# Kernel tuning notes

Hardware: AMD Instinct MI355X
Metric: run time of the kernel (lower is better)

The kernel has to match this reference:

```python
import jax, jax.numpy as jnp
import numpy as np

# Config (matches init_kwargs)
B, N, F, S, T, L = 4, 128, 128, 5, 32, 2
R_MAX = 10.0
AVG_NEI = 16.0
# ell index of each of the 16 spherical-harmonic components (l=0..3)
ELL_IDX = np.array([0] + [1]*3 + [2]*5 + [3]*7)


def _edges(n):
    # fully-connected directed edge list without self loops (static)
    i = np.arange(n)
    s = np.repeat(i, n)
    r = np.tile(i, n)
    m = s != r
    return jnp.asarray(s[m]), jnp.asarray(r[m])


def _sh(u):
    # real spherical harmonics up to ell=3, component normalization, unit input
    x, y, z = u[..., 0], u[..., 1], u[..., 2]
    s3, s5, s15 = 3**0.5, 5**0.5, 15**0.5
    s35_8, s105, s21_8, s7 = (35/8)**0.5, 105**0.5, (21/8)**0.5, 7**0.5
    comps = [jnp.ones_like(x),
             s3*x, s3*y, s3*z,
             s15*x*y, s15*y*z, 0.5*s5*(3*z*z - 1), s15*x*z, 0.5*s15*(x*x - y*y),
             s35_8*y*(3*x*x - y*y), s105*x*y*z, s21_8*y*(5*z*z - 1),
             0.5*s7*z*(5*z*z - 3), s21_8*x*(5*z*z - 1),
             0.5*s105*z*(x*x - y*y), s35_8*x*(x*x - 3*y*y)]
    return jnp.stack(comps, axis=-1)  # (E,16)


def _forward(positions, node_features, global_features, W_embed, b_embed,
             Wr1, br1, Wr2, Wnode, c1, c2, c3, Wmix0, Wmix1, Wg1, Wg2, Wvout):
    n = positions.shape[1]
    senders, receivers = _edges(n)
    ell = jnp.asarray(ELL_IDX)

    def single(pos, nf, te):
        pos0 = pos
        node_attrs = jax.nn.one_hot(nf - 1, S, dtype=pos.dtype)
        h = jnp.concatenate([node_attrs, jnp.tile(te, (n, 1))], axis=-1)
        scal = h @ W_embed + b_embed            # (N,F) scalar node feats
        vec = jnp.zeros((n, F, 3), pos.dtype)   # (N,F,3) vector node feats
        v = pos[receivers] - pos[senders]       # (E,3)
        lng = jnp.sqrt(jnp.sum(v*v, -1, keepdims=True) + 1e-12)  # (E,1)
        env = 0.5*(jnp.cos(jnp.pi*lng/R_MAX) + 1.0)*(lng < R_MAX)  # cutoff from lengths_0
        for i in range(L):
            u = v / lng
            Y = _sh(u)                                            # (E,16)
            Rw = jax.nn.silu(lng @ Wr1[i] + br1[i]) @ Wr2[i]      # radial MLP (E,4F)
            Rw = (Rw * env).reshape(-1, 4, F)                     # (E,4,F)
            z = (scal @ Wnode[i])[senders]                        # (E,F)
            vdot = jnp.einsum('ecd,ed->ec', vec[senders], u)      # (E,F)
            f = z + vdot
            # tensor-product messages (E,16,F)
            M = Rw[:, ell, :] * Y[:, :, None] * f[:, None, :]
            A = jnp.zeros((n, 16, F), pos.dtype).at[receivers].add(M) / AVG_NEI
            # correlation-3 symmetric-contraction gate via per-ell invariants
            nrm = jnp.zeros((n, 4, F), pos.dtype).at[:, ell, :].add(A*A)
            g = 1.0 + c1[i]*nrm + c2[i]*nrm*nrm + c3[i]*nrm*nrm*nrm
            A = A * g[:, ell, :]
            # linear mix to hidden irreps 128x0e + 128x1o
            scal = A[:, 0, :] @ Wmix0[i]                          # (N,F)
            vec = jnp.einsum('nmc,ck->nkm', A[:, 1:4, :], Wmix1[i])  # (N,F,3)
            # nonlinear readout -> equivariant position update
            gate = jax.nn.silu(scal @ Wg1[i]) @ Wg2[i]            # (N,F)
            mbv = jnp.sum(vec * (gate * Wvout[i])[:, :, None], 1) # (N,3)
            pos = pos + mbv
            v = pos[receivers] - pos[senders]
            lng = jnp.sqrt(jnp.sum(v*v, -1, keepdims=True) + 1e-12)
        return pos - pos0  # predicted noise on positions

    return jax.vmap(single)(positions, node_features, global_features)


def setup_inputs() -> dict:
    key = jax.random.key(0)
    ks = jax.random.split(key, 20)
    sc = 0.1
    p = {}
    p['positions'] = jax.random.normal(ks[0], (B, N, 3), jnp.float32)
    p['node_features'] = jax.random.randint(ks[1], (B, N), 1, S + 1).astype(jnp.int32)
    p['global_features'] = jax.random.normal(ks[2], (B, T), jnp.float32)
    p['W_embed'] = jax.random.normal(ks[3], (S + T, F)) * sc
    p['b_embed'] = jnp.zeros((F,))
    p['Wr1'] = jax.random.normal(ks[4], (L, 1, 64)) * sc
    p['br1'] = jnp.zeros((L, 64))
    p['Wr2'] = jax.random.normal(ks[5], (L, 64, 4 * F)) * sc
    p['Wnode'] = jax.random.normal(ks[6], (L, F, F)) * sc
    p['c1'] = jax.random.normal(ks[7], (L, 4, F)) * 0.01
    p['c2'] = jax.random.normal(ks[8], (L, 4, F)) * 0.001
    p['c3'] = jax.random.normal(ks[9], (L, 4, F)) * 0.0001
    p['Wmix0'] = jax.random.normal(ks[10], (L, F, F)) * sc
    p['Wmix1'] = jax.random.normal(ks[11], (L, F, F)) * sc
    p['Wg1'] = jax.random.normal(ks[12], (L, F, 16)) * sc
    p['Wg2'] = jax.random.normal(ks[13], (L, 16, F)) * sc
    p['Wvout'] = jax.random.normal(ks[14], (L, F)) * sc
    return p


def reference(positions, node_features, global_features, W_embed, b_embed,
              Wr1, br1, Wr2, Wnode, c1, c2, c3, Wmix0, Wmix1, Wg1, Wg2, Wvout):
    return _forward(positions, node_features, global_features, W_embed, b_embed,
                    Wr1, br1, Wr2, Wnode, c1, c2, c3, Wmix0, Wmix1, Wg1, Wg2, Wvout)
```

## Files before the change

kernel.cpp:

```cpp
#include <hip/hip_runtime.h>
#include <hip/hip_bf16.h>
#include <math.h>

#define NB 4
#define NN 128
#define NF 128
#define NS 5
#define NT 32
#define NL 2

typedef __hip_bfloat16 bf16;
typedef short bf16x8 __attribute__((ext_vector_type(8)));
typedef float f32x4 __attribute__((ext_vector_type(4)));

typedef const void __attribute__((address_space(1))) gv_t;
typedef void __attribute__((address_space(3))) lv_t;

__device__ __forceinline__ float b2f(const bf16 x) { return __bfloat162float(x); }
__device__ __forceinline__ float fast_rcp(float x) { return __builtin_amdgcn_rcpf(x); }
__device__ __forceinline__ float fast_rsq(float x) { return __builtin_amdgcn_rsqf(x); }
__device__ __forceinline__ float silu_fast(float x) { return x * fast_rcp(1.0f + __expf(-x)); }
__device__ __forceinline__ float ldf(const void* p, int i, int fl) {
  return fl ? b2f(((const bf16*)p)[i]) : ((const float*)p)[i];
}
__device__ __forceinline__ short f2bf(float x) {
  unsigned u = __float_as_uint(x);
  unsigned r = (u + 0x7fffu + ((u >> 16) & 1u)) >> 16;
  return (short)r;
}
__device__ __forceinline__ void gload16(const float4* g, float4* l) {
  __builtin_amdgcn_global_load_lds((gv_t*)g, (lv_t*)l, 16, 0, 0);
}

#define PI_F 3.14159265358979323846f
#define SQRT3_F 1.7320508075688772f

#define POS_OFF 0
#define GF_OFF  1536
#define WE_OFF  1664
#define BE_OFF  6400
#define WR1_OFF 6528
#define BR1_OFF 6656
#define WR2_OFF 6784
#define WN_OFF  72320
#define C1_OFF  105088
#define C2_OFF  106112
#define C3_OFF  107136
#define M0_OFF  108160
#define M1_OFF  140928
#define G1_OFF  173696
#define G2_OFF  177792
#define WV_OFF  181888
#define CVT_TOTAL 182144

__global__ void prep_convert_kernel(
    const void* __restrict__ pos_raw, const int* __restrict__ nfeat,
    const void* __restrict__ gf,  const void* __restrict__ we,
    const void* __restrict__ be,  const void* __restrict__ wr1,
    const void* __restrict__ br1, const void* __restrict__ wr2,
    const void* __restrict__ wn,  const void* __restrict__ c1,
    const void* __restrict__ c2,  const void* __restrict__ c3,
    const void* __restrict__ m0,  const void* __restrict__ m1,
    const void* __restrict__ g1,  const void* __restrict__ g2,
    const void* __restrict__ wv,
    int* __restrict__ flag, float* __restrict__ cvt,
    float* __restrict__ pos_cur, float4* __restrict__ zv,
    float* __restrict__ env, short* __restrict__ pkw)
{
  __shared__ float posB[NN*3];
  __shared__ float scs[NF];
  __shared__ int sbad;
  const int tid = threadIdx.x;
  const int bn  = blockIdx.x;
  const int b   = bn >> 7;
  const int n   = bn & 127;

  if (tid == 0) sbad = 0;
  __syncthreads();
  {
    const bf16* p = (const bf16*)pos_raw;
    int bad = 0;
    for (int i = tid; i < NB*NN*3; i += 256) {
      float v = b2f(p[i]);
      if (!(fabsf(v) <= 1024.0f)) bad = 1;
    }
    if (bad) sbad = 1;
  }
  __syncthreads();
  const int fl = sbad ? 0 : 1;
  if (bn == 0 && tid == 0) *flag = fl;

  for (int i = bn*256 + tid; i < CVT_TOTAL; i += 512*256) {
    const void* src; int j;
    if      (i < GF_OFF)  { src = pos_raw; j = i - POS_OFF; }
    else if (i < WE_OFF)  { src = gf;  j = i - GF_OFF; }
    else if (i < BE_OFF)  { src = we;  j = i - WE_OFF; }
    else if (i < WR1_OFF) { src = be;  j = i - BE_OFF; }
    else if (i < BR1_OFF) { src = wr1; j = i - WR1_OFF; }
    else if (i < WR2_OFF) { src = br1; j = i - BR1_OFF; }
    else if (i < WN_OFF)  { src = wr2; j = i - WR2_OFF; }
    else if (i < C1_OFF)  { src = wn;  j = i - WN_OFF; }
    else if (i < C2_OFF)  { src = c1;  j = i - C1_OFF; }
    else if (i < C3_OFF)  { src = c2;  j = i - C2_OFF; }
    else if (i < M0_OFF)  { src = c3;  j = i - C3_OFF; }
    else if (i < M1_OFF)  { src = m0;  j = i - M0_OFF; }
    else if (i < G1_OFF)  { src = m1;  j = i - M1_OFF; }
    else if (i < G2_OFF)  { src = g1;  j = i - G1_OFF; }
    else if (i < WV_OFF)  { src = g2;  j = i - G2_OFF; }
    else                  { src = wv;  j = i - WV_OFF; }
    cvt[i] = fl ? b2f(((const bf16*)src)[j]) : ((const float*)src)[j];
  }

  if (bn < 16) {
    int gid  = bn*256 + tid;
    int lyr  = gid >> 11;
    int r    = gid & 2047;
    int wv2  = r >> 9;
    int t    = (r >> 7) & 3;
    int ks   = (r >> 6) & 1;
    int lane = r & 63;
    int qq = lane >> 4, nn = lane & 15;
    int col = wv2*64 + t*16 + nn;
    short* dst = pkw + (size_t)gid*8;
    #pragma unroll
    for (int j = 0; j < 8; ++j) {
      int k = ks*32 + qq*8 + j;
      float v = ldf(wr2, lyr*64*512 + k*512 + col, fl);
      if (wv2 >= 2) v *= SQRT3_F;
      dst[j] = f2bf(v);
    }
  }

  for (int i = tid; i < NN*3; i += 256)
    posB[i] = ldf(pos_raw, b*NN*3 + i, fl);
  if (tid < 128) {
    int sp = nfeat[bn] - 1;
    float acc = ldf(we, sp*NF + tid, fl) + ldf(be, tid, fl);
    #pragma unroll 8
    for (int t = 0; t < NT; ++t)
      acc += ldf(gf, b*NT + t, fl) * ldf(we, (NS + t)*NF + tid, fl);
    scs[tid] = acc;
  }
  __syncthreads();

  if (tid < 128) {
    const int f = tid;
    {
      float px = posB[n*3+0], py = posB[n*3+1], pz = posB[n*3+2];
      float vx = px - posB[f*3+0];
      float vy = py - posB[f*3+1];
      float vz = pz - posB[f*3+2];
      float lng = sqrtf(vx*vx + vy*vy + vz*vz + 1e-12f);
      env[bn*NN + f] = (lng < 10.0f) ? 0.5f*(cosf(PI_F*lng*0.1f) + 1.0f) : 0.0f;
    }
    {
      float acc = 0.f;
      if (fl) {
        const bf16* W = (const bf16*)wn;
        #pragma unroll 8
        for (int k = 0; k < NF; ++k) acc += scs[k] * b2f(W[k*NF + f]);
      } else {
        const float* W = (const float*)wn;
        #pragma unroll 8
        for (int k = 0; k < NF; ++k) acc += scs[k] * W[k*NF + f];
      }
      zv[(size_t)bn*NF + f] = make_float4(acc, 0.f, 0.f, 0.f);
    }
    if (f < 3) pos_cur[bn*3 + f] = posB[n*3 + f];
  }
}

__global__ __launch_bounds__(256, 2)
void fused_kernel(const float* __restrict__ posIn, float* __restrict__ posOut,
                  const float4* __restrict__ zvIn, float4* __restrict__ zvOut,
                  const float* __restrict__ env,  const float* __restrict__ cvt,
                  const short* __restrict__ pk, int layer, int last,
                  const int* __restrict__ flag, void* __restrict__ out)
{
  union SM {
    float4 zvp[2][16][NF];
    struct {
      float P[8][32][17];
      float Pg[8][16];
      float scs[NF];
      float h16[16];
      float red[2][4];
    } nd;
  };
  __shared__ __align__(16) SM sm;
  __shared__ float posL[NN*3];
  __shared__ float envL[NN];
  __shared__ float w1L[64], b1L[64];
  __shared__ __align__(16) short hidA[2][16][72];
  __shared__ __align__(16) float4 uenvL[2][16];
  __shared__ float Ash[4][NF];

  const int tid  = threadIdx.x;
  const int bidx = blockIdx.x;
  const int b    = bidx >> 7;
  const int n    = bidx & 127;

  const int wvid  = tid >> 6;
  const int lane  = tid & 63;
  const int n16   = lane & 15;
  const int q     = lane >> 4;
  const int halfB = wvid >> 1;

  {
    const float4* g = zvIn + (size_t)b*NN*NF + wvid*64 + lane;
    float4* l = &sm.zvp[0][0][0] + wvid*64;
    #pragma unroll
    for (int rep = 0; rep < 8; ++rep)
      gload16(g + rep*256, l + rep*256);
  }

  for (int i = tid; i < NN*3; i += 256)
    posL[i] = posIn[b*NN*3 + i];
  if (tid < 128) envL[tid] = env[(size_t)(b*NN + n)*NN + tid];
  if (tid < 64) {
    w1L[tid] = cvt[WR1_OFF + layer*64 + tid];
    b1L[tid] = cvt[BR1_OFF + layer*64 + tid];
  }
  bf16x8 bfr[4][2];
  {
    const bf16x8* PK = (const bf16x8*)pk + (size_t)layer*2048 + wvid*512 + lane;
    #pragma unroll
    for (int t = 0; t < 4; ++t) {
      #pragma unroll
      for (int ks = 0; ks < 2; ++ks)
        bfr[t][ks] = PK[(t*2 + ks)*64];
    }
  }
  float acR[12];
  #pragma unroll
  for (int i = 0; i < 12; ++i) acR[i] = 0.f;

  __syncthreads();

  const float hrx = posL[n*3 + 0];
  const float hry = posL[n*3 + 1];
  const float hrz = posL[n*3 + 2];
  const float w1v = w1L[lane], b1v = b1L[lane];

  #pragma unroll
  for (int j = 0; j < 4; ++j) {
    int si = wvid*4 + j;
    int s  = si;
    float vx = hrx - posL[s*3 + 0];
    float vy = hry - posL[s*3 + 1];
    float vz = hrz - posL[s*3 + 2];
    float d = vx*vx + vy*vy + vz*vz + 1e-12f;
    float lng = d * fast_rsq(d);
    hidA[0][si][lane] = f2bf(silu_fast(lng * w1v + b1v));
  }
  if (tid < 16) {
    int s = tid;
    float vx = hrx - posL[s*3 + 0];
    float vy = hry - posL[s*3 + 1];
    float vz = hrz - posL[s*3 + 2];
    float d = vx*vx + vy*vy + vz*vz + 1e-12f;
    float inv = fast_rsq(d);
    float envw = (s == n) ? 0.f : envL[s] * 0.0625f;
    uenvL[0][tid] = make_float4(vx*inv, vy*inv, vz*inv, envw);
  }
  __syncthreads();

  #pragma unroll 2
  for (int c = 0; c < 8; ++c) {
    const int cb = c & 1, nb = cb ^ 1;
    const int nc0 = (c + 1) * 16;

    if (c < 7) {
      const float4* g = zvIn + ((size_t)b*NN + nc0)*NF + wvid*64 + lane;
      float4* l = &sm.zvp[nb][0][0] + wvid*64;
      #pragma unroll
      for (int rep = 0; rep < 8; ++rep)
        gload16(g + rep*256, l + rep*256);
    }

    bf16x8 af0 = *(const bf16x8*)&hidA[cb][n16][q*8];
    bf16x8 af1 = *(const bf16x8*)&hidA[cb][n16][q*8 + 32];
    float4 ue[4];
    #pragma unroll
    for (int r = 0; r < 4; ++r) ue[r] = uenvL[cb][q*4 + r];

    #pragma unroll
    for (int t = 0; t < 4; ++t) {
      f32x4 Cf = {0.f, 0.f, 0.f, 0.f};
      Cf = __builtin_amdgcn_mfma_f32_16x16x32_bf16(af0, bfr[t][0], Cf, 0, 0, 0);
      Cf = __builtin_amdgcn_mfma_f32_16x16x32_bf16(af1, bfr[t][1], Cf, 0, 0, 0);
      int f = (wvid*64 + t*16 + n16) & 127;
      if (!halfB) {
        float a0 = 0.f;
        #pragma unroll
        for (int r = 0; r < 4; ++r) {
          float4 zv = sm.zvp[cb][q*4 + r][f];
          float fv = zv.x + ue[r].x*zv.y + ue[r].y*zv.z + ue[r].z*zv.w;
          a0 += (Cf[r] * ue[r].w) * fv;
        }
        acR[t] += a0;
      } else {
        float t1 = 0.f, t2 = 0.f, t3 = 0.f;
        #pragma unroll
        for (int r = 0; r < 4; ++r) {
          float4 zv = sm.zvp[cb][q*4 + r][f];
          float fv = zv.x + ue[r].x*zv.y + ue[r].y*zv.z + ue[r].z*zv.w;
          float tt = (Cf[r] * ue[r].w) * fv;
          t1 += tt * ue[r].x;
          t2 += tt * ue[r].y;
          t3 += tt * ue[r].z;
        }
        acR[t*3 + 0] += t1;
        acR[t*3 + 1] += t2;
        acR[t*3 + 2] += t3;
      }
    }

    if (c < 7) {
      #pragma unroll
      for (int j = 0; j < 4; ++j) {
        int si = wvid*4 + j;
        int s  = nc0 + si;
        float vx = hrx - posL[s*3 + 0];
        float vy = hry - posL[s*3 + 1];
        float vz = hrz - posL[s*3 + 2];
        float d = vx*vx + vy*vy + vz*vz + 1e-12f;
        float lng = d * fast_rsq(d);
        hidA[nb][si][lane] = f2bf(silu_fast(lng * w1v + b1v));
      }
      if (tid < 16) {
        int s = nc0 + tid;
        float vx = hrx - posL[s*3 + 0];
        float vy = hry - posL[s*3 + 1];
        float vz = hrz - posL[s*3 + 2];
        float d = vx*vx + vy*vy + vz*vz + 1e-12f;
        float inv = fast_rsq(d);
        float envw = (s == n) ? 0.f : envL[s] * 0.0625f;
        uenvL[nb][tid] = make_float4(vx*inv, vy*inv, vz*inv, envw);
      }
    }
    __syncthreads();
  }

  #pragma unroll
  for (int i = 0; i < 12; ++i) {
    float v = acR[i];
    v += __shfl_xor(v, 16, 64);
    v += __shfl_xor(v, 32, 64);
    acR[i] = v;
  }
  if (lane < 16) {
    #pragma unroll
    for (int t = 0; t < 4; ++t) {
      int f = (wvid*64 + t*16 + lane) & 127;
      if (!halfB) {
        Ash[0][f] = acR[t];
      } else {
        Ash[1][f] = acR[t*3 + 0];
        Ash[2][f] = acR[t*3 + 1];
        Ash[3][f] = acR[t*3 + 2];
      }
    }
  }
  __syncthreads();

  const int fn = tid & 127;
  float v0 = 0.f, v1 = 0.f, v2 = 0.f;
  float zacc = 0.f;

  if (tid < 128) {
    float a0 = Ash[0][fn];
    float a1 = Ash[1][fn];
    float a2 = Ash[2][fn];
    float a3 = Ash[3][fn];
    float n0 = a0*a0;
    float C1 = cvt[C1_OFF + (layer*4 + 0)*NF + fn];
    float C2 = cvt[C2_OFF + (layer*4 + 0)*NF + fn];
    float C3 = cvt[C3_OFF + (layer*4 + 0)*NF + fn];
    float g0 = 1.0f + C1*n0 + C2*n0*n0 + C3*n0*n0*n0;
    float n1 = a1*a1 + a2*a2 + a3*a3;
    float D1 = cvt[C1_OFF + (layer*4 + 1)*NF + fn];
    float D2 = cvt[C2_OFF + (layer*4 + 1)*NF + fn];
    float D3 = cvt[C3_OFF + (layer*4 + 1)*NF + fn];
    float g1 = 1.0f + D1*n1 + D2*n1*n1 + D3*n1*n1*n1;
    Ash[0][fn] = a0 * g0;
    Ash[1][fn] = a1 * g1;
    Ash[2][fn] = a2 * g1;
    Ash[3][fn] = a3 * g1;
  }
  __syncthreads();

  {
    const float* M0 = cvt + M0_OFF + layer*NF*NF;
    const float* M1 = cvt + M1_OFF + layer*NF*NF;
    const int kh = tid >> 5;
    const int fq = tid & 31;
    float s0=0.f,s1=0.f,s2=0.f,s3=0.f;
    float w00=0.f,w01=0.f,w02=0.f,w03=0.f;
    float w10=0.f,w11=0.f,w12=0.f,w13=0.f;
    float w20=0.f,w21=0.f,w22=0.f,w23=0.f;
    #pragma unroll 4
    for (int kk = 0; kk < 16; ++kk) {
      int k = kh*16 + kk;
      float a0 = Ash[0][k], a1 = Ash[1][k], a2 = Ash[2][k], a3 = Ash[3][k];
      float4 m0 = *(const float4*)(M0 + k*NF + fq*4);
      float4 m1 = *(const float4*)(M1 + k*NF + fq*4);
      s0 += a0*m0.x; s1 += a0*m0.y; s2 += a0*m0.z; s3 += a0*m0.w;
      w00 += a1*m1.x; w01 += a1*m1.y; w02 += a1*m1.z; w03 += a1*m1.w;
      w10 += a2*m1.x; w11 += a2*m1.y; w12 += a2*m1.z; w13 += a2*m1.w;
      w20 += a3*m1.x; w21 += a3*m1.y; w22 += a3*m1.z; w23 += a3*m1.w;
    }
    float* Pp = &sm.nd.P[kh][fq][0];
    Pp[0]=s0;  Pp[1]=s1;  Pp[2]=s2;  Pp[3]=s3;
    Pp[4]=w00; Pp[5]=w01; Pp[6]=w02; Pp[7]=w03;
    Pp[8]=w10; Pp[9]=w11; Pp[10]=w12; Pp[11]=w13;
    Pp[12]=w20; Pp[13]=w21; Pp[14]=w22; Pp[15]=w23;
  }
  __syncthreads();

  if (tid < 128) {
    int fq = fn >> 2, j = fn & 3;
    float sn = 0.f;
    #pragma unroll
    for (int kh = 0; kh < 8; ++kh) {
      const float* Pp = &sm.nd.P[kh][fq][0];
      sn += Pp[j];
      v0 += Pp[4 + j];
      v1 += Pp[8 + j];
      v2 += Pp[12 + j];
    }
    sm.nd.scs[fn] = sn;
  }
  __syncthreads();

  if (!last) {
    const float* W = cvt + WN_OFF + (layer+1)*NF*NF;
    const int kh = tid >> 5;
    const int fq = tid & 31;
    float s0=0.f,s1=0.f,s2=0.f,s3=0.f;
    #pragma unroll 4
    for (int kk = 0; kk < 16; ++kk) {
      int k = kh*16 + kk;
      float a = sm.nd.scs[k];
      float4 m = *(const float4*)(W + k*NF + fq*4);
      s0 += a*m.x; s1 += a*m.y; s2 += a*m.z; s3 += a*m.w;
    }
    float* Pp = &sm.nd.P[kh][fq][0];
    Pp[0]=s0; Pp[1]=s1; Pp[2]=s2; Pp[3]=s3;
  }
  if (tid < 128) {
    const float* G1 = cvt + G1_OFF + layer*NF*16;
    int o = tid & 15, g = tid >> 4;
    float acc = 0.f;
    #pragma unroll
    for (int kk = 0; kk < 16; ++kk) {
      int k = g*16 + kk;
      acc += sm.nd.scs[k] * G1[k*16 + o];
    }
    sm.nd.Pg[g][o] = acc;
  }
  __syncthreads();

  if (!last && tid < 128) {
    int fq = fn >> 2, j = fn & 3;
    #pragma unroll
    for (int kh = 0; kh < 8; ++kh) zacc += sm.nd.P[kh][fq][j];
  }
  if (tid < 16) {
    float acc = 0.f;
    #pragma unroll
    for (int g = 0; g < 8; ++g) acc += sm.nd.Pg[g][tid];
    sm.nd.h16[tid] = silu_fast(acc);
  }
  __syncthreads();

  if (tid < 128) {
    const float* G2 = cvt + G2_OFF + layer*16*NF;
    float gate = 0.f;
    #pragma unroll
    for (int j = 0; j < 16; ++j)
      gate += sm.nd.h16[j] * G2[j*NF + fn];
    float gv = gate * cvt[WV_OFF + layer*NF + fn];

    if (!last)
      zvOut[(size_t)bidx*NF + fn] = make_float4(zacc, v0, v1, v2);

    float p0 = v0*gv, p1 = v1*gv, p2 = v2*gv;
    #pragma unroll
    for (int off = 32; off > 0; off >>= 1) {
      p0 += __shfl_down(p0, off, 64);
      p1 += __shfl_down(p1, off, 64);
      p2 += __shfl_down(p2, off, 64);
    }
    int wave = fn >> 6;
    if ((fn & 63) == 0) {
      sm.nd.red[wave][0] = p0;
      sm.nd.red[wave][1] = p1;
      sm.nd.red[wave][2] = p2;
    }
  }
  __syncthreads();
  if (tid == 0) {
    float m0 = sm.nd.red[0][0] + sm.nd.red[1][0];
    float m1 = sm.nd.red[0][1] + sm.nd.red[1][1];
    float m2 = sm.nd.red[0][2] + sm.nd.red[1][2];
    float px = posL[n*3+0] + m0;
    float py = posL[n*3+1] + m1;
    float pz = posL[n*3+2] + m2;
    if (!last) {
      posOut[bidx*3+0] = px;
      posOut[bidx*3+1] = py;
      posOut[bidx*3+2] = pz;
    } else {
      float ox = px - cvt[POS_OFF + bidx*3+0];
      float oy = py - cvt[POS_OFF + bidx*3+1];
      float oz = pz - cvt[POS_OFF + bidx*3+2];
      if (*flag) {
        bf16* o = (bf16*)out;
        o[bidx*3+0] = __float2bfloat16(ox);
        o[bidx*3+1] = __float2bfloat16(oy);
        o[bidx*3+2] = __float2bfloat16(oz);
      } else {
        float* o = (float*)out;
        o[bidx*3+0] = ox;
        o[bidx*3+1] = oy;
        o[bidx*3+2] = oz;
      }
    }
  }
}

extern "C" void kernel_launch(void* const* d_in, const int* in_sizes, int n_in,
                              void* d_out, int out_size, void* d_ws, size_t ws_size,
                              hipStream_t stream)
{
  (void)in_sizes; (void)n_in; (void)out_size; (void)ws_size;
  const int* nfeat = (const int*)d_in[1];

  float*  ws   = (float*)d_ws;
  int*    flag = (int*)ws;
  float*  cvt  = ws + 16;
  float*  pos0 = cvt + CVT_TOTAL;
  float*  pos1 = pos0 + NB*NN*3;
  float4* zv0  = (float4*)(pos1 + NB*NN*3);
  float4* zv1  = zv0 + (size_t)NB*NN*NF;
  float*  env  = (float*)(zv1 + (size_t)NB*NN*NF);
  short*  pk   = (short*)(env + NB*NN*NN);

  prep_convert_kernel<<<512, 256, 0, stream>>>(
      d_in[0], nfeat, d_in[2], d_in[3], d_in[4], d_in[5], d_in[6], d_in[7],
      d_in[8], d_in[9], d_in[10], d_in[11], d_in[12], d_in[13], d_in[14],
      d_in[15], d_in[16], flag, cvt, pos0, zv0, env, pk);

  fused_kernel<<<512, 256, 0, stream>>>(pos0, pos1, zv0, zv1, env, cvt, pk,
                                        0, 0, flag, d_out);
  fused_kernel<<<512, 256, 0, stream>>>(pos1, (float*)0, zv1, (float4*)0, env,
                                        cvt, pk, 1, 1, flag, d_out);
}
```

Measured before the change: 141.8 us.

## Merge prep and both layer kernels into one persistent kernel with grid barriers

Replaces the three launches (prep plus two layer kernels) with a single kernel that synchronises all 512 blocks through an atomic-counter grid barrier between stages. The envelope and positions are kept in shared memory instead of round-tripping through global buffers, and the barrier counter is reset with a memset each call. This targets launch overhead and inter-kernel gaps. It adds the cost of spinning barriers and depends on all 512 blocks being co-resident (launch_bounds 256,2); if they are not, the kernel deadlocks.

```diff
diff --git a/kernel.cpp b/kernel.cpp
--- a/kernel.cpp
+++ b/kernel.cpp
@@ -30,6 +30,18 @@
 }
 __device__ __forceinline__ void gload16(const float4* g, float4* l) {
   __builtin_amdgcn_global_load_lds((gv_t*)g, (lv_t*)l, 16, 0, 0);
+}
+
+__device__ __forceinline__ void grid_barrier(unsigned* bar, unsigned target) {
+  __syncthreads();
+  if (threadIdx.x == 0) {
+    __threadfence();
+    __hip_atomic_fetch_add(bar, 1u, __ATOMIC_RELAXED, __HIP_MEMORY_SCOPE_AGENT);
+    while (__hip_atomic_load(bar, __ATOMIC_RELAXED, __HIP_MEMORY_SCOPE_AGENT) < target)
+      __builtin_amdgcn_s_sleep(2);
+    __threadfence();
+  }
+  __syncthreads();
 }
 
 #define PI_F 3.14159265358979323846f
@@ -53,7 +65,8 @@
 #define WV_OFF  181888
 #define CVT_TOTAL 182144
 
-__global__ void prep_convert_kernel(
+__global__ __launch_bounds__(256, 2)
+void mega_kernel(
     const void* __restrict__ pos_raw, const int* __restrict__ nfeat,
     const void* __restrict__ gf,  const void* __restrict__ we,
     const void* __restrict__ be,  const void* __restrict__ wr1,
@@ -63,17 +76,40 @@
     const void* __restrict__ m0,  const void* __restrict__ m1,
     const void* __restrict__ g1,  const void* __restrict__ g2,
     const void* __restrict__ wv,
-    int* __restrict__ flag, float* __restrict__ cvt,
-    float* __restrict__ pos_cur, float4* __restrict__ zv,
-    float* __restrict__ env, short* __restrict__ pkw)
+    unsigned* __restrict__ bar, float* __restrict__ cvt,
+    float* __restrict__ pos1, float4* __restrict__ zv0,
+    float4* __restrict__ zv1, short* __restrict__ pkw,
+    void* __restrict__ out)
 {
-  __shared__ float posB[NN*3];
-  __shared__ float scs[NF];
+  union SM {
+    float4 zvp[2][16][NF];
+    struct {
+      float P[8][32][17];
+      float Pg[8][16];
+      float scs[NF];
+      float h16[16];
+      float red[2][4];
+    } nd;
+  };
+  __shared__ __align__(16) SM sm;
+  __shared__ float posL[NN*3];
+  __shared__ float envL[NN];
+  __shared__ float w1L[64], b1L[64];
+  __shared__ __align__(16) short hidA[2][16][72];
+  __shared__ __align__(16) float4 uenvL[2][16];
+  __shared__ float Ash[4][NF];
   __shared__ int sbad;
-  const int tid = threadIdx.x;
-  const int bn  = blockIdx.x;
-  const int b   = bn >> 7;
-  const int n   = bn & 127;
+
+  const int tid  = threadIdx.x;
+  const int bidx = blockIdx.x;
+  const int b    = bidx >> 7;
+  const int n    = bidx & 127;
+
+  const int wvid  = tid >> 6;
+  const int lane  = tid & 63;
+  const int n16   = lane & 15;
+  const int q     = lane >> 4;
+  const int halfB = wvid >> 1;
 
   if (tid == 0) sbad = 0;
   __syncthreads();
@@ -88,9 +124,11 @@
   }
   __syncthreads();
   const int fl = sbad ? 0 : 1;
-  if (bn == 0 && tid == 0) *flag = fl;
-
-  for (int i = bn*256 + tid; i < CVT_TOTAL; i += 512*256) {
+
+  for (int i = tid; i < NN*3; i += 256)
+    posL[i] = ldf(pos_raw, b*NN*3 + i, fl);
+
+  for (int i = bidx*256 + tid; i < CVT_TOTAL; i += 512*256) {
     const void* src; int j;
     if      (i < GF_OFF)  { src = pos_raw; j = i - POS_OFF; }
     else if (i < WE_OFF)  { src = gf;  j = i - GF_OFF; }
@@ -111,15 +149,15 @@
     cvt[i] = fl ? b2f(((const bf16*)src)[j]) : ((const float*)src)[j];
   }
 
-  if (bn < 16) {
-    int gid  = bn*256 + tid;
+  if (bidx < 16) {
+    int gid  = bidx*256 + tid;
     int lyr  = gid >> 11;
     int r    = gid & 2047;
     int wv2  = r >> 9;
     int t    = (r >> 7) & 3;
     int ks   = (r >> 6) & 1;
-    int lane = r & 63;
-    int qq = lane >> 4, nn = lane & 15;
+    int ln   = r & 63;
+    int qq = ln >> 4, nn = ln & 15;
     int col = wv2*64 + t*16 + nn;
     short* dst = pkw + (size_t)gid*8;
     #pragma unroll
@@ -131,402 +169,372 @@
     }
   }
 
-  for (int i = tid; i < NN*3; i += 256)
-    posB[i] = ldf(pos_raw, b*NN*3 + i, fl);
   if (tid < 128) {
-    int sp = nfeat[bn] - 1;
+    int sp = nfeat[bidx] - 1;
     float acc = ldf(we, sp*NF + tid, fl) + ldf(be, tid, fl);
     #pragma unroll 8
     for (int t = 0; t < NT; ++t)
       acc += ldf(gf, b*NT + t, fl) * ldf(we, (NS + t)*NF + tid, fl);
-    scs[tid] = acc;
+    sm.nd.scs[tid] = acc;
   }
   __syncthreads();
 
   if (tid < 128) {
     const int f = tid;
     {
-      float px = posB[n*3+0], py = posB[n*3+1], pz = posB[n*3+2];
-      float vx = px - posB[f*3+0];
-      float vy = py - posB[f*3+1];
-      float vz = pz - posB[f*3+2];
+      float px = posL[n*3+0], py = posL[n*3+1], pz = posL[n*3+2];
+      float vx = px - posL[f*3+0];
+      float vy = py - posL[f*3+1];
+      float vz = pz - posL[f*3+2];
       float lng = sqrtf(vx*vx + vy*vy + vz*vz + 1e-12f);
-      env[bn*NN + f] = (lng < 10.0f) ? 0.5f*(cosf(PI_F*lng*0.1f) + 1.0f) : 0.0f;
+      envL[f] = (lng < 10.0f) ? 0.5f*(cosf(PI_F*lng*0.1f) + 1.0f) : 0.0f;
     }
     {
       float acc = 0.f;
       if (fl) {
         const bf16* W = (const bf16*)wn;
         #pragma unroll 8
-        for (int k = 0; k < NF; ++k) acc += scs[k] * b2f(W[k*NF + f]);
+        for (int k = 0; k < NF; ++k) acc += sm.nd.scs[k] * b2f(W[k*NF + f]);
       } else {
         const float* W = (const float*)wn;
         #pragma unroll 8
-        for (int k = 0; k < NF; ++k) acc += scs[k] * W[k*NF + f];
-      }
-      zv[(size_t)bn*NF + f] = make_float4(acc, 0.f, 0.f, 0.f);
-    }
-    if (f < 3) pos_cur[bn*3 + f] = posB[n*3 + f];
-  }
-}
-
-__global__ __launch_bounds__(256, 2)
-void fused_kernel(const float* __restrict__ posIn, float* __restrict__ posOut,
-                  const float4* __restrict__ zvIn, float4* __restrict__ zvOut,
-                  const float* __restrict__ env,  const float* __restrict__ cvt,
-                  const short* __restrict__ pk, int layer, int last,
-                  const int* __restrict__ flag, void* __restrict__ out)
-{
-  union SM {
-    float4 zvp[2][16][NF];
-    struct {
-      float P[8][32][17];
-      float Pg[8][16];
-      float scs[NF];
-      float h16[16];
-      float red[2][4];
-    } nd;
-  };
-  __shared__ __align__(16) SM sm;
-  __shared__ float posL[NN*3];
-  __shared__ float envL[NN];
-  __shared__ float w1L[64], b1L[64];
-  __shared__ __align__(16) short hidA[2][16][72];
-  __shared__ __align__(16) float4 uenvL[2][16];
-  __shared__ float Ash[4][NF];
-
-  const int tid  = threadIdx.x;
-  const int bidx = blockIdx.x;
-  const int b    = bidx >> 7;
-  const int n    = bidx & 127;
-
-  const int wvid  = tid >> 6;
-  const int lane  = tid & 63;
-  const int n16   = lane & 15;
-  const int q     = lane >> 4;
-  const int halfB = wvid >> 1;
-
-  {
-    const float4* g = zvIn + (size_t)b*NN*NF + wvid*64 + lane;
-    float4* l = &sm.zvp[0][0][0] + wvid*64;
-    #pragma unroll
-    for (int rep = 0; rep < 8; ++rep)
-      gload16(g + rep*256, l + rep*256);
-  }
-
-  for (int i = tid; i < NN*3; i += 256)
-    posL[i] = posIn[b*NN*3 + i];
-  if (tid < 128) envL[tid] = env[(size_t)(b*NN + n)*NN + tid];
-  if (tid < 64) {
-    w1L[tid] = cvt[WR1_OFF + layer*64 + tid];
-    b1L[tid] = cvt[BR1_OFF + layer*64 + tid];
-  }
-  bf16x8 bfr[4][2];
-  {
-    const bf16x8* PK = (const bf16x8*)pk + (size_t)layer*2048 + wvid*512 + lane;
-    #pragma unroll
-    for (int t = 0; t < 4; ++t) {
-      #pragma unroll
-      for (int ks = 0; ks < 2; ++ks)
-        bfr[t][ks] = PK[(t*2 + ks)*64];
-    }
-  }
-  float acR[12];
-  #pragma unroll
-  for (int i = 0; i < 12; ++i) acR[i] = 0.f;
-
-  __syncthreads();
-
-  const float hrx = posL[n*3 + 0];
-  const float hry = posL[n*3 + 1];
-  const float hrz = posL[n*3 + 2];
-  const float w1v = w1L[lane], b1v = b1L[lane];
-
-  #pragma unroll
-  for (int j = 0; j < 4; ++j) {
-    int si = wvid*4 + j;
-    int s  = si;
-    float vx = hrx - posL[s*3 + 0];
-    float vy = hry - posL[s*3 + 1];
-    float vz = hrz - posL[s*3 + 2];
-    float d = vx*vx + vy*vy + vz*vz + 1e-12f;
-    float lng = d * fast_rsq(d);
-    hidA[0][si][lane] = f2bf(silu_fast(lng * w1v + b1v));
-  }
-  if (tid < 16) {
-    int s = tid;
-    float vx = hrx - posL[s*3 + 0];
-    float vy = hry - posL[s*3 + 1];
-    float vz = hrz - posL[s*3 + 2];
-    float d = vx*vx + vy*vy + vz*vz + 1e-12f;
-    float inv = fast_rsq(d);
-    float envw = (s == n) ? 0.f : envL[s] * 0.0625f;
-    uenvL[0][tid] = make_float4(vx*inv, vy*inv, vz*inv, envw);
-  }
-  __syncthreads();
-
-  #pragma unroll 2
-  for (int c = 0; c < 8; ++c) {
-    const int cb = c & 1, nb = cb ^ 1;
-    const int nc0 = (c + 1) * 16;
-
-    if (c < 7) {
-      const float4* g = zvIn + ((size_t)b*NN + nc0)*NF + wvid*64 + lane;
-      float4* l = &sm.zvp[nb][0][0] + wvid*64;
+        for (int k = 0; k < NF; ++k) acc += sm.nd.scs[k] * W[k*NF + f];
+      }
+      zv0[(size_t)bidx*NF + f] = make_float4(acc, 0.f, 0.f, 0.f);
+    }
+  }
+
+  grid_barrier(bar, 512);
+
+  for (int layer = 0; layer < NL; ++layer) {
+    const int last = (layer == NL-1);
+    const float4* zvIn  = layer ? zv1 : zv0;
+    float4*       zvOut = layer ? (float4*)0 : zv1;
+
+    if (layer) {
+      grid_barrier(bar, 1024);
+      for (int i = tid; i < NN*3; i += 256)
+        posL[i] = pos1[b*NN*3 + i];
+    }
+    {
+      const float4* g = zvIn + (size_t)b*NN*NF + wvid*64 + lane;
+      float4* l = &sm.zvp[0][0][0] + wvid*64;
       #pragma unroll
       for (int rep = 0; rep < 8; ++rep)
         gload16(g + rep*256, l + rep*256);
     }
-
-    bf16x8 af0 = *(const bf16x8*)&hidA[cb][n16][q*8];
-    bf16x8 af1 = *(const bf16x8*)&hidA[cb][n16][q*8 + 32];
-    float4 ue[4];
+    if (tid < 64) {
+      w1L[tid] = cvt[WR1_OFF + layer*64 + tid];
+      b1L[tid] = cvt[BR1_OFF + layer*64 + tid];
+    }
+    bf16x8 bfr[4][2];
+    {
+      const bf16x8* PK = (const bf16x8*)pkw + (size_t)layer*2048 + wvid*512 + lane;
+      #pragma unroll
+      for (int t = 0; t < 4; ++t) {
+        #pragma unroll
+        for (int ks = 0; ks < 2; ++ks)
+          bfr[t][ks] = PK[(t*2 + ks)*64];
+      }
+    }
+    float acR[12];
     #pragma unroll
-    for (int r = 0; r < 4; ++r) ue[r] = uenvL[cb][q*4 + r];
+    for (int i = 0; i < 12; ++i) acR[i] = 0.f;
+
+    __syncthreads();
+
+    const float hrx = posL[n*3 + 0];
+    const float hry = posL[n*3 + 1];
+    const float hrz = posL[n*3 + 2];
+    const float w1v = w1L[lane], b1v = b1L[lane];
 
     #pragma unroll
-    for (int t = 0; t < 4; ++t) {
-      f32x4 Cf = {0.f, 0.f, 0.f, 0.f};
-      Cf = __builtin_amdgcn_mfma_f32_16x16x32_bf16(af0, bfr[t][0], Cf, 0, 0, 0);
-      Cf = __builtin_amdgcn_mfma_f32_16x16x32_bf16(af1, bfr[t][1], Cf, 0, 0, 0);
-      int f = (wvid*64 + t*16 + n16) & 127;
-      if (!halfB) {
-        float a0 = 0.f;
+    for (int j = 0; j < 4; ++j) {
+      int si = wvid*4 + j;
+      int s  = si;
+      float vx = hrx - posL[s*3 + 0];
+      float vy = hry - posL[s*3 + 1];
+      float vz = hrz - posL[s*3 + 2];
+      float d = vx*vx + vy*vy + vz*vz + 1e-12f;
+      float lng = d * fast_rsq(d);
+      hidA[0][si][lane] = f2bf(silu_fast(lng * w1v + b1v));
+    }
+    if (tid < 16) {
+      int s = tid;
+      float vx = hrx - posL[s*3 + 0];
+      float vy = hry - posL[s*3 + 1];
+      float vz = hrz - posL[s*3 + 2];
+      float d = vx*vx + vy*vy + vz*vz + 1e-12f;
+      float inv = fast_rsq(d);
+      float envw = (s == n) ? 0.f : envL[s] * 0.0625f;
+      uenvL[0][tid] = make_float4(vx*inv, vy*inv, vz*inv, envw);
+    }
+    __syncthreads();
+
+    #pragma unroll 2
+    for (int c = 0; c < 8; ++c) {
+      const int cb = c & 1, nb = cb ^ 1;
+      const int nc0 = (c + 1) * 16;
+
+      if (c < 7) {
+        const float4* g = zvIn + ((size_t)b*NN + nc0)*NF + wvid*64 + lane;
+        float4* l = &sm.zvp[nb][0][0] + wvid*64;
         #pragma unroll
-        for (int r = 0; r < 4; ++r) {
-          float4 zv = sm.zvp[cb][q*4 + r][f];
-          float fv = zv.x + ue[r].x*zv.y + ue[r].y*zv.z + ue[r].z*zv.w;
-          a0 += (Cf[r] * ue[r].w) * fv;
+        for (int rep = 0; rep < 8; ++rep)
+          gload16(g + rep*256, l + rep*256);
+      }
+
+      bf16x8 af0 = *(const bf16x8*)&hidA[cb][n16][q*8];
+      bf16x8 af1 = *(const bf16x8*)&hidA[cb][n16][q*8 + 32];
+      float4 ue[4];
+      #pragma unroll
+      for (int r = 0; r < 4; ++r) ue[r] = uenvL[cb][q*4 + r];
+
+      #pragma unroll
+      for (int t = 0; t < 4; ++t) {
+        f32x4 Cf = {0.f, 0.f, 0.f, 0.f};
+        Cf = __builtin_amdgcn_mfma_f32_16x16x32_bf16(af0, bfr[t][0], Cf, 0, 0, 0);
+        Cf = __builtin_amdgcn_mfma_f32_16x16x32_bf16(af1, bfr[t][1], Cf, 0, 0, 0);
+        int f = (wvid*64 + t*16 + n16) & 127;
+        if (!halfB) {
+          float a0 = 0.f;
+          #pragma unroll
+          for (int r = 0; r < 4; ++r) {
+            float4 zv = sm.zvp[cb][q*4 + r][f];
+            float fv = zv.x + ue[r].x*zv.y + ue[r].y*zv.z + ue[r].z*zv.w;
+            a0 += (Cf[r] * ue[r].w) * fv;
+          }
+          acR[t] += a0;
+        } else {
+          float t1 = 0.f, t2 = 0.f, t3 = 0.f;
+          #pragma unroll
+          for (int r = 0; r < 4; ++r) {
+            float4 zv = sm.zvp[cb][q*4 + r][f];
+            float fv = zv.x + ue[r].x*zv.y + ue[r].y*zv.z + ue[r].z*zv.w;
+            float tt = (Cf[r] * ue[r].w) * fv;
+            t1 += tt * ue[r].x;
+            t2 += tt * ue[r].y;
+            t3 += tt * ue[r].z;
+          }
+          acR[t*3 + 0] += t1;
+          acR[t*3 + 1] += t2;
+          acR[t*3 + 2] += t3;
         }
-        acR[t] += a0;
+      }
+
+      if (c < 7) {
+        #pragma unroll
+        for (int j = 0; j < 4; ++j) {
+          int si = wvid*4 + j;
+          int s  = nc0 + si;
+          float vx = hrx - posL[s*3 + 0];
+          float vy = hry - posL[s*3 + 1];
+          float vz = hrz - posL[s*3 + 2];
+          float d = vx*vx + vy*vy + vz*vz + 1e-12f;
+          float lng = d * fast_rsq(d);
+          hidA[nb][si][lane] = f2bf(silu_fast(lng * w1v + b1v));
+        }
+        if (tid < 16) {
+          int s = nc0 + tid;
+          float vx = hrx - posL[s*3 + 0];
+          float vy = hry - posL[s*3 + 1];
+          float vz = hrz - posL[s*3 + 2];
+          float d = vx*vx + vy*vy + vz*vz + 1e-12f;
+          float inv = fast_rsq(d);
+          float envw = (s == n) ? 0.f : envL[s] * 0.0625f;
+          uenvL[nb][tid] = make_float4(vx*inv, vy*inv, vz*inv, envw);
+        }
+      }
+      __syncthreads();
+    }
+
+    #pragma unroll
+    for (int i = 0; i < 12; ++i) {
+      float v = acR[i];
+      v += __shfl_xor(v, 16, 64);
+      v += __shfl_xor(v, 32, 64);
+      acR[i] = v;
+    }
+    if (lane < 16) {
+      #pragma unroll
+      for (int t = 0; t < 4; ++t) {
+        int f = (wvid*64 + t*16 + lane) & 127;
+        if (!halfB) {
+          Ash[0][f] = acR[t];
+        } else {
+          Ash[1][f] = acR[t*3 + 0];
+          Ash[2][f] = acR[t*3 + 1];
+          Ash[3][f] = acR[t*3 + 2];
+        }
+      }
+    }
+    __syncthreads();
+
+    const int fn = tid & 127;
+    float v0 = 0.f, v1 = 0.f, v2 = 0.f;
+    float zacc = 0.f;
+
+    if (tid < 128) {
+      float a0 = Ash[0][fn];
+      float a1 = Ash[1][fn];
+      float a2 = Ash[2][fn];
+      float a3 = Ash[3][fn];
+      float n0 = a0*a0;
+      float C1 = cvt[C1_OFF + (layer*4 + 0)*NF + fn];
+      float C2 = cvt[C2_OFF + (layer*4 + 0)*NF + fn];
+      float C3 = cvt[C3_OFF + (layer*4 + 0)*NF + fn];
+      float g0 = 1.0f + C1*n0 + C2*n0*n0 + C3*n0*n0*n0;
+      float n1 = a1*a1 + a2*a2 + a3*a3;
+      float D1 = cvt[C1_OFF + (layer*4 + 1)*NF + fn];
+      float D2 = cvt[C2_OFF + (layer*4 + 1)*NF + fn];
+      float D3 = cvt[C3_OFF + (layer*4 + 1)*NF + fn];
+      float g1 = 1.0f + D1*n1 + D2*n1*n1 + D3*n1*n1*n1;
+      Ash[0][fn] = a0 * g0;
+      Ash[1][fn] = a1 * g1;
+      Ash[2][fn] = a2 * g1;
+      Ash[3][fn] = a3 * g1;
+    }
+    __syncthreads();
+
+    {
+      const float* M0 = cvt + M0_OFF + layer*NF*NF;
+      const float* M1 = cvt + M1_OFF + layer*NF*NF;
+      const int kh = tid >> 5;
+      const int fq = tid & 31;
+      float s0=0.f,s1=0.f,s2=0.f,s3=0.f;
+      float w00=0.f,w01=0.f,w02=0.f,w03=0.f;
+      float w10=0.f,w11=0.f,w12=0.f,w13=0.f;
+      float w20=0.f,w21=0.f,w22=0.f,w23=0.f;
+      #pragma unroll 4
+      for (int kk = 0; kk < 16; ++kk) {
+        int k = kh*16 + kk;
+        float a0 = Ash[0][k], a1 = Ash[1][k], a2 = Ash[2][k], a3 = Ash[3][k];
+        float4 mm0 = *(const float4*)(M0 + k*NF + fq*4);
+        float4 mm1 = *(const float4*)(M1 + k*NF + fq*4);
+        s0 += a0*mm0.x; s1 += a0*mm0.y; s2 += a0*mm0.z; s3 += a0*mm0.w;
+        w00 += a1*mm1.x; w01 += a1*mm1.y; w02 += a1*mm1.z; w03 += a1*mm1.w;
+        w10 += a2*mm1.x; w11 += a2*mm1.y; w12 += a2*mm1.z; w13 += a2*mm1.w;
+        w20 += a3*mm1.x; w21 += a3*mm1.y; w22 += a3*mm1.z; w23 += a3*mm1.w;
+      }
+      float* Pp = &sm.nd.P[kh][fq][0];
+      Pp[0]=s0;  Pp[1]=s1;  Pp[2]=s2;  Pp[3]=s3;
+      Pp[4]=w00; Pp[5]=w01; Pp[6]=w02; Pp[7]=w03;
+      Pp[8]=w10; Pp[9]=w11; Pp[10]=w12; Pp[11]=w13;
+      Pp[12]=w20; Pp[13]=w21; Pp[14]=w22; Pp[15]=w23;
+    }
+    __syncthreads();
+
+    if (tid < 128) {
+      int fq = fn >> 2, j = fn & 3;
+      float sn = 0.f;
+      #pragma unroll
+      for (int kh = 0; kh < 8; ++kh) {
+        const float* Pp = &sm.nd.P[kh][fq][0];
+        sn += Pp[j];
+        v0 += Pp[4 + j];
+        v1 += Pp[8 + j];
+        v2 += Pp[12 + j];
+      }
+      sm.nd.scs[fn] = sn;
+    }
+    __syncthreads();
+
+    if (!last) {
+      const float* W = cvt + WN_OFF + (layer+1)*NF*NF;
+      const int kh = tid >> 5;
+      const int fq = tid & 31;
+      float s0=0.f,s1=0.f,s2=0.f,s3=0.f;
+      #pragma unroll 4
+      for (int kk = 0; kk < 16; ++kk) {
+        int k = kh*16 + kk;
+        float a = sm.nd.scs[k];
+        float4 m = *(const float4*)(W + k*NF + fq*4);
+        s0 += a*m.x; s1 += a*m.y; s2 += a*m.z; s3 += a*m.w;
+      }
+      float* Pp = &sm.nd.P[kh][fq][0];
+      Pp[0]=s0; Pp[1]=s1; Pp[2]=s2; Pp[3]=s3;
+    }
+    if (tid < 128) {
+      const float* G1 = cvt + G1_OFF + layer*NF*16;
+      int o = tid & 15, g = tid >> 4;
+      float acc = 0.f;
+      #pragma unroll
+      for (int kk = 0; kk < 16; ++kk) {
+        int k = g*16 + kk;
+        acc += sm.nd.scs[k] * G1[k*16 + o];
+      }
+      sm.nd.Pg[g][o] = acc;
+    }
+    __syncthreads();
+
+    if (!last && tid < 128) {
+      int fq = fn >> 2, j = fn & 3;
+      #pragma unroll
+      for (int kh = 0; kh < 8; ++kh) zacc += sm.nd.P[kh][fq][j];
+    }
+    if (tid < 16) {
+      float acc = 0.f;
+      #pragma unroll
+      for (int g = 0; g < 8; ++g) acc += sm.nd.Pg[g][tid];
+      sm.nd.h16[tid] = silu_fast(acc);
+    }
+    __syncthreads();
+
+    if (tid < 128) {
+      const float* G2 = cvt + G2_OFF + layer*16*NF;
+      float gate = 0.f;
+      #pragma unroll
+      for (int j = 0; j < 16; ++j)
+        gate += sm.nd.h16[j] * G2[j*NF + fn];
+      float gv = gate * cvt[WV_OFF + layer*NF + fn];
+
+      if (!last)
+        zvOut[(size_t)bidx*NF + fn] = make_float4(zacc, v0, v1, v2);
+
+      float p0 = v0*gv, p1 = v1*gv, p2 = v2*gv;
+      #pragma unroll
+      for (int off = 32; off > 0; off >>= 1) {
+        p0 += __shfl_down(p0, off, 64);
+        p1 += __shfl_down(p1, off, 64);
+        p2 += __shfl_down(p2, off, 64);
+      }
+      int wave = fn >> 6;
+      if ((fn & 63) == 0) {
+        sm.nd.red[wave][0] = p0;
+        sm.nd.red[wave][1] = p1;
+        sm.nd.red[wave][2] = p2;
+      }
+    }
+    __syncthreads();
+    if (tid == 0) {
+      float m0r = sm.nd.red[0][0] + sm.nd.red[1][0];
+      float m1r = sm.nd.red[0][1] + sm.nd.red[1][1];
+      float m2r = sm.nd.red[0][2] + sm.nd.red[1][2];
+      float px = posL[n*3+0] + m0r;
+      float py = posL[n*3+1] + m1r;
+      float pz = posL[n*3+2] + m2r;
+      if (!last) {
+        pos1[bidx*3+0] = px;
+        pos1[bidx*3+1] = py;
+        pos1[bidx*3+2] = pz;
       } else {
-        float t1 = 0.f, t2 = 0.f, t3 = 0.f;
-        #pragma unroll
-        for (int r = 0; r < 4; ++r) {
-          float4 zv = sm.zvp[cb][q*4 + r][f];
-          float fv = zv.x + ue[r].x*zv.y + ue[r].y*zv.z + ue[r].z*zv.w;
-          float tt = (Cf[r] * ue[r].w) * fv;
-          t1 += tt * ue[r].x;
-          t2 += tt * ue[r].y;
-          t3 += tt * ue[r].z;
+        float ox = px - cvt[POS_OFF + bidx*3+0];
+        float oy = py - cvt[POS_OFF + bidx*3+1];
+        float oz = pz - cvt[POS_OFF + bidx*3+2];
+        if (fl) {
+          bf16* o = (bf16*)out;
+          o[bidx*3+0] = __float2bfloat16(ox);
+          o[bidx*3+1] = __float2bfloat16(oy);
+          o[bidx*3+2] = __float2bfloat16(oz);
+        } else {
+          float* o = (float*)out;
+          o[bidx*3+0] = ox;
+          o[bidx*3+1] = oy;
+          o[bidx*3+2] = oz;
         }
-        acR[t*3 + 0] += t1;
-        acR[t*3 + 1] += t2;
-        acR[t*3 + 2] += t3;
-      }
-    }
-
-    if (c < 7) {
-      #pragma unroll
-      for (int j = 0; j < 4; ++j) {
-        int si = wvid*4 + j;
-        int s  = nc0 + si;
-        float vx = hrx - posL[s*3 + 0];
-        float vy = hry - posL[s*3 + 1];
-        float vz = hrz - posL[s*3 + 2];
-        float d = vx*vx + vy*vy + vz*vz + 1e-12f;
-        float lng = d * fast_rsq(d);
-        hidA[nb][si][lane] = f2bf(silu_fast(lng * w1v + b1v));
-      }
-      if (tid < 16) {
-        int s = nc0 + tid;
-        float vx = hrx - posL[s*3 + 0];
-        float vy = hry - posL[s*3 + 1];
-        float vz = hrz - posL[s*3 + 2];
-        float d = vx*vx + vy*vy + vz*vz + 1e-12f;
-        float inv = fast_rsq(d);
-        float envw = (s == n) ? 0.f : envL[s] * 0.0625f;
-        uenvL[nb][tid] = make_float4(vx*inv, vy*inv, vz*inv, envw);
-      }
-    }
-    __syncthreads();
-  }
-
-  #pragma unroll
-  for (int i = 0; i < 12; ++i) {
-    float v = acR[i];
-    v += __shfl_xor(v, 16, 64);
-    v += __shfl_xor(v, 32, 64);
-    acR[i] = v;
-  }
-  if (lane < 16) {
-    #pragma unroll
-    for (int t = 0; t < 4; ++t) {
-      int f = (wvid*64 + t*16 + lane) & 127;
-      if (!halfB) {
-        Ash[0][f] = acR[t];
-      } else {
-        Ash[1][f] = acR[t*3 + 0];
-        Ash[2][f] = acR[t*3 + 1];
-        Ash[3][f] = acR[t*3 + 2];
-      }
-    }
-  }
-  __syncthreads();
-
-  const int fn = tid & 127;
-  float v0 = 0.f, v1 = 0.f, v2 = 0.f;
-  float zacc = 0.f;
-
-  if (tid < 128) {
-    float a0 = Ash[0][fn];
-    float a1 = Ash[1][fn];
-    float a2 = Ash[2][fn];
-    float a3 = Ash[3][fn];
-    float n0 = a0*a0;
-    float C1 = cvt[C1_OFF + (layer*4 + 0)*NF + fn];
-    float C2 = cvt[C2_OFF + (layer*4 + 0)*NF + fn];
-    float C3 = cvt[C3_OFF + (layer*4 + 0)*NF + fn];
-    float g0 = 1.0f + C1*n0 + C2*n0*n0 + C3*n0*n0*n0;
-    float n1 = a1*a1 + a2*a2 + a3*a3;
-    float D1 = cvt[C1_OFF + (layer*4 + 1)*NF + fn];
-    float D2 = cvt[C2_OFF + (layer*4 + 1)*NF + fn];
-    float D3 = cvt[C3_OFF + (layer*4 + 1)*NF + fn];
-    float g1 = 1.0f + D1*n1 + D2*n1*n1 + D3*n1*n1*n1;
-    Ash[0][fn] = a0 * g0;
-    Ash[1][fn] = a1 * g1;
-    Ash[2][fn] = a2 * g1;
-    Ash[3][fn] = a3 * g1;
-  }
-  __syncthreads();
-
-  {
-    const float* M0 = cvt + M0_OFF + layer*NF*NF;
-    const float* M1 = cvt + M1_OFF + layer*NF*NF;
-    const int kh = tid >> 5;
-    const int fq = tid & 31;
-    float s0=0.f,s1=0.f,s2=0.f,s3=0.f;
-    float w00=0.f,w01=0.f,w02=0.f,w03=0.f;
-    float w10=0.f,w11=0.f,w12=0.f,w13=0.f;
-    float w20=0.f,w21=0.f,w22=0.f,w23=0.f;
-    #pragma unroll 4
-    for (int kk = 0; kk < 16; ++kk) {
-      int k = kh*16 + kk;
-      float a0 = Ash[0][k], a1 = Ash[1][k], a2 = Ash[2][k], a3 = Ash[3][k];
-      float4 m0 = *(const float4*)(M0 + k*NF + fq*4);
-      float4 m1 = *(const float4*)(M1 + k*NF + fq*4);
-      s0 += a0*m0.x; s1 += a0*m0.y; s2 += a0*m0.z; s3 += a0*m0.w;
-      w00 += a1*m1.x; w01 += a1*m1.y; w02 += a1*m1.z; w03 += a1*m1.w;
-      w10 += a2*m1.x; w11 += a2*m1.y; w12 += a2*m1.z; w13 += a2*m1.w;
-      w20 += a3*m1.x; w21 += a3*m1.y; w22 += a3*m1.z; w23 += a3*m1.w;
-    }
-    float* Pp = &sm.nd.P[kh][fq][0];
-    Pp[0]=s0;  Pp[1]=s1;  Pp[2]=s2;  Pp[3]=s3;
-    Pp[4]=w00; Pp[5]=w01; Pp[6]=w02; Pp[7]=w03;
-    Pp[8]=w10; Pp[9]=w11; Pp[10]=w12; Pp[11]=w13;
-    Pp[12]=w20; Pp[13]=w21; Pp[14]=w22; Pp[15]=w23;
-  }
-  __syncthreads();
-
-  if (tid < 128) {
-    int fq = fn >> 2, j = fn & 3;
-    float sn = 0.f;
-    #pragma unroll
-    for (int kh = 0; kh < 8; ++kh) {
-      const float* Pp = &sm.nd.P[kh][fq][0];
-      sn += Pp[j];
-      v0 += Pp[4 + j];
-      v1 += Pp[8 + j];
-      v2 += Pp[12 + j];
-    }
-    sm.nd.scs[fn] = sn;
-  }
-  __syncthreads();
-
-  if (!last) {
-    const float* W = cvt + WN_OFF + (layer+1)*NF*NF;
-    const int kh = tid >> 5;
-    const int fq = tid & 31;
-    float s0=0.f,s1=0.f,s2=0.f,s3=0.f;
-    #pragma unroll 4
-    for (int kk = 0; kk < 16; ++kk) {
-      int k = kh*16 + kk;
-      float a = sm.nd.scs[k];
-      float4 m = *(const float4*)(W + k*NF + fq*4);
-      s0 += a*m.x; s1 += a*m.y; s2 += a*m.z; s3 += a*m.w;
-    }
-    float* Pp = &sm.nd.P[kh][fq][0];
-    Pp[0]=s0; Pp[1]=s1; Pp[2]=s2; Pp[3]=s3;
-  }
-  if (tid < 128) {
-    const float* G1 = cvt + G1_OFF + layer*NF*16;
-    int o = tid & 15, g = tid >> 4;
-    float acc = 0.f;
-    #pragma unroll
-    for (int kk = 0; kk < 16; ++kk) {
-      int k = g*16 + kk;
-      acc += sm.nd.scs[k] * G1[k*16 + o];
-    }
-    sm.nd.Pg[g][o] = acc;
-  }
-  __syncthreads();
-
-  if (!last && tid < 128) {
-    int fq = fn >> 2, j = fn & 3;
-    #pragma unroll
-    for (int kh = 0; kh < 8; ++kh) zacc += sm.nd.P[kh][fq][j];
-  }
-  if (tid < 16) {
-    float acc = 0.f;
-    #pragma unroll
-    for (int g = 0; g < 8; ++g) acc += sm.nd.Pg[g][tid];
-    sm.nd.h16[tid] = silu_fast(acc);
-  }
-  __syncthreads();
-
-  if (tid < 128) {
-    const float* G2 = cvt + G2_OFF + layer*16*NF;
-    float gate = 0.f;
-    #pragma unroll
-    for (int j = 0; j < 16; ++j)
-      gate += sm.nd.h16[j] * G2[j*NF + fn];
-    float gv = gate * cvt[WV_OFF + layer*NF + fn];
-
-    if (!last)
-      zvOut[(size_t)bidx*NF + fn] = make_float4(zacc, v0, v1, v2);
-
-    float p0 = v0*gv, p1 = v1*gv, p2 = v2*gv;
-    #pragma unroll
-    for (int off = 32; off > 0; off >>= 1) {
-      p0 += __shfl_down(p0, off, 64);
-      p1 += __shfl_down(p1, off, 64);
-      p2 += __shfl_down(p2, off, 64);
-    }
-    int wave = fn >> 6;
-    if ((fn & 63) == 0) {
-      sm.nd.red[wave][0] = p0;
-      sm.nd.red[wave][1] = p1;
-      sm.nd.red[wave][2] = p2;
-    }
-  }
-  __syncthreads();
-  if (tid == 0) {
-    float m0 = sm.nd.red[0][0] + sm.nd.red[1][0];
-    float m1 = sm.nd.red[0][1] + sm.nd.red[1][1];
-    float m2 = sm.nd.red[0][2] + sm.nd.red[1][2];
-    float px = posL[n*3+0] + m0;
-    float py = posL[n*3+1] + m1;
-    float pz = posL[n*3+2] + m2;
-    if (!last) {
-      posOut[bidx*3+0] = px;
-      posOut[bidx*3+1] = py;
-      posOut[bidx*3+2] = pz;
-    } else {
-      float ox = px - cvt[POS_OFF + bidx*3+0];
-      float oy = py - cvt[POS_OFF + bidx*3+1];
-      float oz = pz - cvt[POS_OFF + bidx*3+2];
-      if (*flag) {
-        bf16* o = (bf16*)out;
-        o[bidx*3+0] = __float2bfloat16(ox);
-        o[bidx*3+1] = __float2bfloat16(oy);
-        o[bidx*3+2] = __float2bfloat16(oz);
-      } else {
-        float* o = (float*)out;
-        o[bidx*3+0] = ox;
-        o[bidx*3+1] = oy;
-        o[bidx*3+2] = oz;
-      }
-    }
+      }
+    }
+    __syncthreads();
   }
 }
 
@@ -537,23 +545,18 @@
   (void)in_sizes; (void)n_in; (void)out_size; (void)ws_size;
   const int* nfeat = (const int*)d_in[1];
 
-  float*  ws   = (float*)d_ws;
-  int*    flag = (int*)ws;
-  float*  cvt  = ws + 16;
-  float*  pos0 = cvt + CVT_TOTAL;
-  float*  pos1 = pos0 + NB*NN*3;
-  float4* zv0  = (float4*)(pos1 + NB*NN*3);
-  float4* zv1  = zv0 + (size_t)NB*NN*NF;
-  float*  env  = (float*)(zv1 + (size_t)NB*NN*NF);
-  short*  pk   = (short*)(env + NB*NN*NN);
-
-  prep_convert_kernel<<<512, 256, 0, stream>>>(
+  float*    ws   = (float*)d_ws;
+  unsigned* bar  = (unsigned*)ws;
+  float*    cvt  = ws + 16;
+  float*    pos1 = cvt + CVT_TOTAL;
+  float4*   zv0  = (float4*)(pos1 + NB*NN*3);
+  float4*   zv1  = zv0 + (size_t)NB*NN*NF;
+  short*    pk   = (short*)(zv1 + (size_t)NB*NN*NF);
+
+  hipMemsetAsync(bar, 0, 16, stream);
+
+  mega_kernel<<<512, 256, 0, stream>>>(
       d_in[0], nfeat, d_in[2], d_in[3], d_in[4], d_in[5], d_in[6], d_in[7],
       d_in[8], d_in[9], d_in[10], d_in[11], d_in[12], d_in[13], d_in[14],
-      d_in[15], d_in[16], flag, cvt, pos0, zv0, env, pk);
-
-  fused_kernel<<<512, 256, 0, stream>>>(pos0, pos1, zv0, zv1, env, cvt, pk,
-                                        0, 0, flag, d_out);
-  fused_kernel<<<512, 256, 0, stream>>>(pos1, (float*)0, zv1, (float4*)0, env,
-                                        cvt, pk, 1, 1, flag, d_out);
+      d_in[15], d_in[16], bar, cvt, pos1, zv0, zv1, pk, d_out);
 }
```

New measurement: 227.4 us. 60.3% more time.
